# Performance work log

Hardware: AMD Instinct MI355X
Metric: run time of the kernel (lower is better)

Reference implementation:

```python
import jax, jax.numpy as jnp
import numpy as np

B, P, C = 8, 8192, 91            # images, proposals/image, classes (incl. background)
PRE_NMS_TOPK = 1000              # fixed-size candidate set per image for NMS
DET_PER_IMG = 100                # detections_per_img
SCORE_THRESH = 0.05
NMS_THRESH = 0.5
MIN_SIZE = 0.01                  # remove_small_boxes min_size
BBOX_W = (10.0, 10.0, 5.0, 5.0)  # bbox_reg_weights
BBOX_XFORM_CLIP = float(np.log(1000.0 / 16.0))
NEG = -1e9


def setup_inputs() -> dict:
    key = jax.random.key(0)
    k1, k2, k3, k4, k5, k6 = jax.random.split(key, 6)
    H, W = 800, 1333
    class_logits = jax.random.normal(k1, (B, P, C), jnp.float32)
    box_regression = jax.random.normal(k2, (B, P, 4 * C), jnp.float32) * 0.5
    # random valid proposal boxes inside the image
    cx = jax.random.uniform(k3, (B, P)) * W
    cy = jax.random.uniform(k4, (B, P)) * H
    bw = jax.random.uniform(k5, (B, P)) * 200.0 + 16.0
    bh = jax.random.uniform(k6, (B, P)) * 200.0 + 16.0
    x1 = jnp.clip(cx - 0.5 * bw, 0.0, W - 1.0)
    y1 = jnp.clip(cy - 0.5 * bh, 0.0, H - 1.0)
    x2 = jnp.clip(cx + 0.5 * bw, x1 + 1.0, float(W))
    y2 = jnp.clip(cy + 0.5 * bh, y1 + 1.0, float(H))
    proposals = jnp.stack([x1, y1, x2, y2], axis=-1)
    image_hw = jnp.array([H, W], jnp.int32)
    return {"class_logits": class_logits, "box_regression": box_regression,
            "proposals": proposals, "image_hw": image_hw}


def _iou_matrix(b):
    # b: [K,4] -> [K,K] pairwise IoU
    area = (b[:, 2] - b[:, 0]) * (b[:, 3] - b[:, 1])
    lt = jnp.maximum(b[:, None, :2], b[None, :, :2])
    rb = jnp.minimum(b[:, None, 2:], b[None, :, 2:])
    wh = jnp.clip(rb - lt, 0.0)
    inter = wh[..., 0] * wh[..., 1]
    return inter / (area[:, None] + area[None, :] - inter + 1e-9)


def _postprocess(class_logits, box_regression, proposals, image_hw):
    Hf = image_hw[0].astype(jnp.float32)
    Wf = image_hw[1].astype(jnp.float32)
    wx, wy, ww, wh = BBOX_W
    # --- BoxCoder.decode ---
    widths = proposals[..., 2] - proposals[..., 0]            # [B,P]
    heights = proposals[..., 3] - proposals[..., 1]
    ctr_x = proposals[..., 0] + 0.5 * widths
    ctr_y = proposals[..., 1] + 0.5 * heights
    rel = box_regression.reshape(B, P, C, 4)
    dx = rel[..., 0] / wx
    dy = rel[..., 1] / wy
    dw = jnp.minimum(rel[..., 2] / ww, BBOX_XFORM_CLIP)
    dh = jnp.minimum(rel[..., 3] / wh, BBOX_XFORM_CLIP)
    pcx = dx * widths[..., None] + ctr_x[..., None]           # [B,P,C]
    pcy = dy * heights[..., None] + ctr_y[..., None]
    pw = jnp.exp(dw) * widths[..., None]
    ph = jnp.exp(dh) * heights[..., None]
    # --- clip_boxes_to_image ---
    x1 = jnp.clip(pcx - 0.5 * pw, 0.0, Wf)
    y1 = jnp.clip(pcy - 0.5 * ph, 0.0, Hf)
    x2 = jnp.clip(pcx + 0.5 * pw, 0.0, Wf)
    y2 = jnp.clip(pcy + 0.5 * ph, 0.0, Hf)
    boxes = jnp.stack([x1, y1, x2, y2], axis=-1)              # [B,P,C,4]
    scores = jax.nn.softmax(class_logits, axis=-1)            # [B,P,C]
    # drop background class 0, flatten (proposal, class) candidates
    M = P * (C - 1)
    boxes_f = boxes[:, :, 1:, :].reshape(B, M, 4)
    scores_f = scores[:, :, 1:].reshape(B, M)
    labels_f = jnp.broadcast_to(jnp.tile(jnp.arange(1, C, dtype=jnp.int32), P), (B, M))
    # score threshold + remove_small_boxes as score masking (fixed shapes)
    ws = boxes_f[..., 2] - boxes_f[..., 0]
    hs = boxes_f[..., 3] - boxes_f[..., 1]
    valid = (scores_f > SCORE_THRESH) & (ws >= MIN_SIZE) & (hs >= MIN_SIZE)
    mscores = jnp.where(valid, scores_f, NEG)
    offset_scale = jnp.maximum(Hf, Wf) + 1.0

    def per_image(b, s, l):
        # pre-NMS top-k candidates (sorted descending, matching NMS score order)
        sk, idx = jax.lax.top_k(s, PRE_NMS_TOPK)              # [K]
        bk = b[idx]                                           # [K,4]
        lk = l[idx]
        valid_k = sk > NEG / 2
        # batched_nms via per-class coordinate offsets
        bo = bk + (lk.astype(jnp.float32) * offset_scale)[:, None]
        iou = _iou_matrix(bo)                                 # [K,K]
        K = PRE_NMS_TOPK
        rng = jnp.arange(K)
        def body(i, supp):
            active = jnp.logical_and(jnp.logical_not(supp[i]), valid_k[i])
            new = active & (iou[i] > NMS_THRESH) & (rng > i)
            return supp | new
        supp = jax.lax.fori_loop(0, K, body, jnp.zeros((K,), bool))
        keep = jnp.logical_and(jnp.logical_not(supp), valid_k)
        fs = jnp.where(keep, sk, NEG)
        fsd, fidx = jax.lax.top_k(fs, DET_PER_IMG)
        fb = bk[fidx]
        fl = lk[fidx]
        ok = fsd > NEG / 2
        return (jnp.where(ok[:, None], fb, 0.0),
                jnp.where(ok, fsd, 0.0),
                jnp.where(ok, fl, 0))

    return jax.vmap(per_image)(boxes_f, mscores, labels_f)


def reference(class_logits, box_regression, proposals, image_hw):
    boxes, scores, labels = _postprocess(class_logits, box_regression, proposals, image_hw)
    return boxes, scores, labels  # [B,100,4] float, [B,100] float, [B,100] int32
```

## Files before the change

kernel.cpp:

```cpp
#include <hip/hip_runtime.h>

namespace {

constexpr int NB = 8, NP = 8192, NC = 91;
constexpr int KTOP = 1000, NDET = 100;
constexpr int MROWS = 1024;
constexpr int NBUCK = 4096, SORTN = 4096;
constexpr int NLAB = 90;
constexpr int SHARDS = 32;
constexpr int SHCAP = 4864;
constexpr float SCORE_T = 0.05f;
constexpr float MIN_SZ = 0.01f;
constexpr float NMS_T = 0.5f;
constexpr float CLIPV = 4.135166556742356f;
constexpr float NEGV = -1e9f;

typedef unsigned long long ull;

__device__ __forceinline__ void decode_box(const float4& pr, const float4& rel,
                                           float Wf, float Hf,
                                           float& x1, float& y1, float& x2, float& y2) {
  float w = pr.z - pr.x, h = pr.w - pr.y;
  float cx = pr.x + 0.5f * w, cy = pr.y + 0.5f * h;
  float dx = rel.x / 10.0f, dy = rel.y / 10.0f;
  float dw = fminf(rel.z / 5.0f, CLIPV), dh = fminf(rel.w / 5.0f, CLIPV);
  float pcx = dx * w + cx, pcy = dy * h + cy;
  float pw = expf(dw) * w, ph = expf(dh) * h;
  x1 = fminf(fmaxf(pcx - 0.5f * pw, 0.0f), Wf);
  y1 = fminf(fmaxf(pcy - 0.5f * ph, 0.0f), Hf);
  x2 = fminf(fmaxf(pcx + 0.5f * pw, 0.0f), Wf);
  y2 = fminf(fmaxf(pcy + 0.5f * ph, 0.0f), Hf);
}

__device__ __forceinline__ int score_bucket(unsigned bits) {
  return min((int)((bits - 0x3D000000u) >> 14), NBUCK - 1);
}

__global__ __launch_bounds__(256) void k_candidates(
    const float* __restrict__ logits, const float* __restrict__ boxreg,
    const float* __restrict__ props, const int* __restrict__ hw,
    ull* __restrict__ dense, int* __restrict__ shcnt) {
  __shared__ float sh[16 * NC];
  __shared__ ull stage[16][20];
  __shared__ int gcnt[16];
  __shared__ int gbase[16];
  int tid = threadIdx.x;
  int base = blockIdx.x * 16;
  const float4* src4 = reinterpret_cast<const float4*>(logits + (size_t)base * NC);
  float4* sh4 = reinterpret_cast<float4*>(sh);
  for (int i = tid; i < (16 * NC) / 4; i += 256) sh4[i] = src4[i];
  __syncthreads();

  int lane = tid & 63;
  int l16 = lane & 15;
  int grp = lane >> 4;
  int wv = tid >> 6;
  int lp = wv * 4 + grp;
  int gw = base + lp;
  int b = gw >> 13;
  int p = gw & (NP - 1);
  float Hf = (float)hw[0], Wf = (float)hw[1];
  const float* row = sh + lp * NC;

  float zreg[6];
  float m = -3.0e38f;
#pragma unroll
  for (int k = 0; k < 6; ++k) {
    int c = k * 16 + l16;
    float z = (c < NC) ? row[c] : -3.0e38f;
    zreg[k] = z;
    m = fmaxf(m, z);
  }
#pragma unroll
  for (int d = 1; d < 16; d <<= 1) m = fmaxf(m, __shfl_xor(m, d, 64));
  float S = 0.0f;
#pragma unroll
  for (int k = 0; k < 6; ++k) {
    int c = k * 16 + l16;
    S += (c < NC) ? expf(zreg[k] - m) : 0.0f;
  }
#pragma unroll
  for (int d = 1; d < 16; d <<= 1) S += __shfl_xor(S, d, 64);

  float invS = 1.0f / S;
  float thr = m + logf(SCORE_T * S) - 1e-3f;

  float4 pr = reinterpret_cast<const float4*>(props)[gw];
  const float4* relrow = reinterpret_cast<const float4*>(boxreg + (size_t)gw * 4 * NC);
  unsigned below = (1u << l16) - 1u;
  int n = 0;
#pragma unroll
  for (int k = 0; k < 6; ++k) {
    int c = k * 16 + l16;
    bool ok = (c >= 1) && (c < NC) && (zreg[k] > thr);
    float sc = 0.0f;
    if (ok) {
      sc = expf(zreg[k] - m) * invS;
      ok = sc > SCORE_T;
      if (ok) {
        float4 rel = relrow[c];
        float x1, y1, x2, y2;
        decode_box(pr, rel, Wf, Hf, x1, y1, x2, y2);
        ok = ((x2 - x1) >= MIN_SZ) && ((y2 - y1) >= MIN_SZ);
      }
    }
    ull bal = __ballot(ok);
    unsigned gm = (unsigned)((bal >> (grp * 16)) & 0xFFFFull);
    if (ok) {
      int pos = n + __popc(gm & below);
      unsigned bits = __float_as_uint(sc);
      int idx = p * (NC - 1) + (c - 1);
      if (pos < 20) stage[lp][pos] = ((ull)bits << 32) | (unsigned)(~(unsigned)idx);
    }
    n += __popc(gm);
  }
  if (l16 == 0) gcnt[lp] = min(n, 20);
  __syncthreads();
  int shard = blockIdx.x & (SHARDS - 1);
  if (tid == 0) {
    int off[16];
    int tot = 0;
#pragma unroll
    for (int g = 0; g < 16; ++g) { off[g] = tot; tot += gcnt[g]; }
    int bs = tot ? atomicAdd(&shcnt[b * SHARDS + shard], tot) : 0;
#pragma unroll
    for (int g = 0; g < 16; ++g) gbase[g] = bs + off[g];
  }
  __syncthreads();
  ull* dst = dense + (size_t)(b * SHARDS + shard) * SHCAP;
  for (int j = l16; j < gcnt[lp]; j += 16) dst[gbase[lp] + j] = stage[lp][j];
}

__global__ __launch_bounds__(1024) void k_select(
    const ull* __restrict__ dense, const int* __restrict__ shcnt,
    const float* __restrict__ boxreg, const float* __restrict__ props,
    const int* __restrict__ hw,
    float* __restrict__ topk_score, float* __restrict__ det_box,
    int* __restrict__ det_label, int* __restrict__ keep, int* __restrict__ nvalid) {
  __shared__ int h[NBUCK];
  __shared__ int cur[NBUCK];
  __shared__ ull sk[SORTN];
  __shared__ int sbs;
  int b = blockIdx.x, tid = threadIdx.x;
#pragma unroll
  for (int k = 0; k < NBUCK / 1024; ++k) h[tid + k * 1024] = 0;
  if (tid == 0) sbs = 0;
  __syncthreads();
  for (int s = 0; s < SHARDS; ++s) {
    int cnt = shcnt[b * SHARDS + s];
    const ull* seg = dense + (size_t)(b * SHARDS + s) * SHCAP;
    for (int i = tid; i < cnt; i += 1024)
      atomicAdd(&h[score_bucket((unsigned)(seg[i] >> 32))], 1);
  }
  __syncthreads();
  for (int d = 1; d < NBUCK; d <<= 1) {
    int v[NBUCK / 1024];
#pragma unroll
    for (int k = 0; k < NBUCK / 1024; ++k) {
      int i = tid + k * 1024;
      v[k] = h[i] + ((i + d < NBUCK) ? h[i + d] : 0);
    }
    __syncthreads();
#pragma unroll
    for (int k = 0; k < NBUCK / 1024; ++k) h[tid + k * 1024] = v[k];
    __syncthreads();
  }
#pragma unroll
  for (int k = 0; k < NBUCK / 1024; ++k) {
    int i = tid + k * 1024;
    if (h[i] >= KTOP && (i == NBUCK - 1 || h[i + 1] < KTOP)) sbs = i;
  }
  __syncthreads();
#pragma unroll
  for (int k = 0; k < NBUCK / 1024; ++k) {
    int i = tid + k * 1024;
    cur[i] = (i + 1 < NBUCK) ? h[i + 1] : 0;
  }
  __syncthreads();
  int sb = sbs;
  int total = min(h[sb], SORTN);
  for (int s = 0; s < SHARDS; ++s) {
    int cnt = shcnt[b * SHARDS + s];
    const ull* seg = dense + (size_t)(b * SHARDS + s) * SHCAP;
    for (int i = tid; i < cnt; i += 1024) {
      ull key = seg[i];
      int bk = score_bucket((unsigned)(key >> 32));
      if (bk < sb) continue;
      int pos = atomicAdd(&cur[bk], 1);
      if (pos < SORTN) sk[pos] = key;
    }
  }
  __syncthreads();
  float Hf = (float)hw[0], Wf = (float)hw[1];
  for (int i = tid; i < total; i += 1024) {
    ull key = sk[i];
    int bk = score_bucket((unsigned)(key >> 32));
    int s0 = (bk + 1 < NBUCK) ? h[bk + 1] : 0;
    int e = min(cur[bk], total);
    int r = s0;
    for (int j = s0; j < e; ++j) r += (sk[j] > key) ? 1 : 0;
    if (r < KTOP) {
      int og = b * KTOP + r;
      topk_score[og] = __uint_as_float((unsigned)(key >> 32));
      int fidx = (int)(~(unsigned)key);
      int p = fidx / (NC - 1), c = fidx % (NC - 1) + 1;
      float4 pr = reinterpret_cast<const float4*>(props)[b * NP + p];
      float4 rel =
          reinterpret_cast<const float4*>(boxreg + (size_t)(b * NP + p) * 4 * NC)[c];
      float x1, y1, x2, y2;
      decode_box(pr, rel, Wf, Hf, x1, y1, x2, y2);
      det_box[(size_t)og * 4 + 0] = x1;
      det_box[(size_t)og * 4 + 1] = y1;
      det_box[(size_t)og * 4 + 2] = x2;
      det_box[(size_t)og * 4 + 3] = y2;
      det_label[og] = c;
      keep[og] = 1;
    }
  }
  int valid_n = min(total, KTOP);
  for (int r = valid_n + tid; r < KTOP; r += 1024) {
    int og = b * KTOP + r;
    topk_score[og] = NEGV;
    det_box[(size_t)og * 4 + 0] = 0.0f;
    det_box[(size_t)og * 4 + 1] = 0.0f;
    det_box[(size_t)og * 4 + 2] = 0.0f;
    det_box[(size_t)og * 4 + 3] = 0.0f;
    det_label[og] = 0;
    keep[og] = 0;
  }
  if (tid == 0) nvalid[b] = valid_n;
}

__global__ __launch_bounds__(64) void k_nms(
    const int* __restrict__ nvalid, const float* __restrict__ det_box,
    const int* __restrict__ det_label, int* __restrict__ keep) {
  __shared__ int list[MROWS];
  __shared__ float4 mbx[64];
  __shared__ unsigned char sup[MROWS];
  int bb = blockIdx.x;
  int b = bb / NLAB;
  int lab = bb % NLAB + 1;
  int lane = threadIdx.x;
  int nv = nvalid[b];
  ull below = (1ull << lane) - 1ull;
  const int* ll = det_label + b * KTOP;
  int c = 0;
  for (int base = 0; base < KTOP; base += 64) {
    int i = base + lane;
    bool mb = (i < KTOP) && (i < nv) && (ll[i] == lab);
    ull bal = __ballot(mb);
    if (mb) list[c + __popcll(bal & below)] = i;
    c += __popcll(bal);
  }
  if (c <= 1) return;
  __syncthreads();
  const float4* bbx = reinterpret_cast<const float4*>(det_box) + (size_t)b * KTOP;
  if (c <= 64) {
    if (lane < c) mbx[lane] = bbx[list[lane]];
    __syncthreads();
    float4 bx = mbx[(lane < c) ? lane : 0];
    float area = (bx.z - bx.x) * (bx.w - bx.y);
    ull col = 0ull;
    for (int i = 0; i + 1 < c; ++i) {
      float4 bi = mbx[i];
      float ai = (bi.z - bi.x) * (bi.w - bi.y);
      float ltx = fmaxf(bi.x, bx.x), lty = fmaxf(bi.y, bx.y);
      float rbx = fminf(bi.z, bx.z), rby = fminf(bi.w, bx.w);
      float iw = fmaxf(rbx - ltx, 0.0f), ih = fmaxf(rby - lty, 0.0f);
      float inter = iw * ih;
      float iou = inter / (ai + area - inter + 1e-9f);
      if ((lane > i) && (lane < c) && (iou > NMS_T)) col |= (1ull << i);
    }
    if (__ballot(col != 0ull)) {
      unsigned s = 0u;
      for (int i = 0; i + 1 < c; ++i) {
        ull act = __ballot(s == 0u);
        s |= (unsigned)((act >> i) & (col >> i) & 1ull);
      }
      if (lane < c && s) keep[b * KTOP + list[lane]] = 0;
    }
  } else {
    if (lane == 0) {
      for (int a = 0; a < c; ++a) sup[a] = 0;
      for (int a = 0; a < c; ++a) {
        if (sup[a]) continue;
        float4 bi = bbx[list[a]];
        float ai = (bi.z - bi.x) * (bi.w - bi.y);
        for (int e = a + 1; e < c; ++e) {
          if (sup[e]) continue;
          float4 bj = bbx[list[e]];
          float aj = (bj.z - bj.x) * (bj.w - bj.y);
          float ltx = fmaxf(bi.x, bj.x), lty = fmaxf(bi.y, bj.y);
          float rbx = fminf(bi.z, bj.z), rby = fminf(bi.w, bj.w);
          float iw = fmaxf(rbx - ltx, 0.0f), ih = fmaxf(rby - lty, 0.0f);
          float inter = iw * ih;
          if (inter / (ai + aj - inter + 1e-9f) > NMS_T) sup[e] = 1;
        }
      }
      for (int a = 0; a < c; ++a)
        if (sup[a]) keep[b * KTOP + list[a]] = 0;
    }
  }
}

__global__ __launch_bounds__(256) void k_output(
    const float* __restrict__ topk_score, const float* __restrict__ det_box,
    const int* __restrict__ det_label, const int* __restrict__ keep,
    float* __restrict__ out) {
  __shared__ int kp[MROWS];
  __shared__ int pf[MROWS];
  int b = blockIdx.x, tid = threadIdx.x;
  for (int i = tid; i < MROWS; i += 256) {
    int v = (i < KTOP) ? keep[b * KTOP + i] : 0;
    kp[i] = v;
    pf[i] = v;
  }
  __syncthreads();
  for (int d = 1; d < MROWS; d <<= 1) {
    int v[4];
#pragma unroll
    for (int k = 0; k < 4; ++k) {
      int i = tid + k * 256;
      v[k] = pf[i] + ((i >= d) ? pf[i - d] : 0);
    }
    __syncthreads();
#pragma unroll
    for (int k = 0; k < 4; ++k) pf[tid + k * 256] = v[k];
    __syncthreads();
  }
  int total = min(pf[KTOP - 1], NDET);
  float* ob = out;
  float* os = out + (size_t)NB * NDET * 4;
  float* ol = os + (size_t)NB * NDET;
  for (int i = tid; i < KTOP; i += 256) {
    if (kp[i]) {
      int r = pf[i] - 1;
      if (r < NDET) {
        ob[((size_t)b * NDET + r) * 4 + 0] = det_box[((size_t)b * KTOP + i) * 4 + 0];
        ob[((size_t)b * NDET + r) * 4 + 1] = det_box[((size_t)b * KTOP + i) * 4 + 1];
        ob[((size_t)b * NDET + r) * 4 + 2] = det_box[((size_t)b * KTOP + i) * 4 + 2];
        ob[((size_t)b * NDET + r) * 4 + 3] = det_box[((size_t)b * KTOP + i) * 4 + 3];
        os[b * NDET + r] = topk_score[b * KTOP + i];
        ol[b * NDET + r] = (float)det_label[b * KTOP + i];
      }
    }
  }
  for (int r = total + tid; r < NDET; r += 256) {
    ob[((size_t)b * NDET + r) * 4 + 0] = 0.0f;
    ob[((size_t)b * NDET + r) * 4 + 1] = 0.0f;
    ob[((size_t)b * NDET + r) * 4 + 2] = 0.0f;
    ob[((size_t)b * NDET + r) * 4 + 3] = 0.0f;
    os[b * NDET + r] = 0.0f;
    ol[b * NDET + r] = 0.0f;
  }
}

}

extern "C" void kernel_launch(void* const* d_in, const int* in_sizes, int n_in,
                              void* d_out, int out_size, void* d_ws, size_t ws_size,
                              hipStream_t stream) {
  const float* logits = (const float*)d_in[0];
  const float* boxreg = (const float*)d_in[1];
  const float* props = (const float*)d_in[2];
  const int* hw = (const int*)d_in[3];

  char* ws = (char*)d_ws;
  size_t off = 0;
  auto alloc = [&](size_t bytes) -> void* {
    void* p = ws + off;
    off += (bytes + 255) & ~(size_t)255;
    return p;
  };
  ull* dense = (ull*)alloc((size_t)NB * SHARDS * SHCAP * 8);
  int* shcnt = (int*)alloc((size_t)NB * SHARDS * 4);
  float* topk_score = (float*)alloc((size_t)NB * KTOP * 4);
  float* det_box = (float*)alloc((size_t)NB * KTOP * 16);
  int* det_label = (int*)alloc((size_t)NB * KTOP * 4);
  int* keep = (int*)alloc((size_t)NB * KTOP * 4);
  int* nvalid = (int*)alloc(NB * 4);

  hipMemsetAsync(shcnt, 0, (size_t)NB * SHARDS * 4, stream);
  k_candidates<<<(NB * NP) / 16, 256, 0, stream>>>(logits, boxreg, props, hw,
                                                   dense, shcnt);
  k_select<<<NB, 1024, 0, stream>>>(dense, shcnt, boxreg, props, hw,
                                    topk_score, det_box, det_label, keep, nvalid);
  k_nms<<<NB * NLAB, 64, 0, stream>>>(nvalid, det_box, det_label, keep);
  k_output<<<NB, 256, 0, stream>>>(topk_score, det_box, det_label, keep, (float*)d_out);
}
```

Baseline: 77.59 us.

## Replace atomic shard compaction with per-block fixed-slot candidate buffers

Each candidate block now writes its survivors into its own fixed-capacity slot and records a per-block count, instead of reserving space in 32 shared shards per image with global atomics. This removes the global atomicAdd contention and the memset launch. In the select kernel, each pair of threads now walks one block's segment, replacing the loop over shards. The trade-off is uneven per-thread work in k_select, since segment counts vary, and reads that are less coalesced than contiguous shard scans.

```diff
diff --git a/kernel.cpp b/kernel.cpp
--- a/kernel.cpp
+++ b/kernel.cpp
@@ -7,8 +7,8 @@
 constexpr int MROWS = 1024;
 constexpr int NBUCK = 4096, SORTN = 4096;
 constexpr int NLAB = 90;
-constexpr int SHARDS = 32;
-constexpr int SHCAP = 4864;
+constexpr int BPI = 512;
+constexpr int BCAP = 304;
 constexpr float SCORE_T = 0.05f;
 constexpr float MIN_SZ = 0.01f;
 constexpr float NMS_T = 0.5f;
@@ -39,7 +39,7 @@
 __global__ __launch_bounds__(256) void k_candidates(
     const float* __restrict__ logits, const float* __restrict__ boxreg,
     const float* __restrict__ props, const int* __restrict__ hw,
-    ull* __restrict__ dense, int* __restrict__ shcnt) {
+    ull* __restrict__ dense, int* __restrict__ bcnt) {
   __shared__ float sh[16 * NC];
   __shared__ ull stage[16][20];
   __shared__ int gcnt[16];
@@ -57,7 +57,6 @@
   int wv = tid >> 6;
   int lp = wv * 4 + grp;
   int gw = base + lp;
-  int b = gw >> 13;
   int p = gw & (NP - 1);
   float Hf = (float)hw[0], Wf = (float)hw[1];
   const float* row = sh + lp * NC;
@@ -116,23 +115,22 @@
   }
   if (l16 == 0) gcnt[lp] = min(n, 20);
   __syncthreads();
-  int shard = blockIdx.x & (SHARDS - 1);
   if (tid == 0) {
     int off[16];
     int tot = 0;
 #pragma unroll
     for (int g = 0; g < 16; ++g) { off[g] = tot; tot += gcnt[g]; }
-    int bs = tot ? atomicAdd(&shcnt[b * SHARDS + shard], tot) : 0;
-#pragma unroll
-    for (int g = 0; g < 16; ++g) gbase[g] = bs + off[g];
-  }
-  __syncthreads();
-  ull* dst = dense + (size_t)(b * SHARDS + shard) * SHCAP;
+#pragma unroll
+    for (int g = 0; g < 16; ++g) gbase[g] = off[g];
+    bcnt[blockIdx.x] = tot;
+  }
+  __syncthreads();
+  ull* dst = dense + (size_t)blockIdx.x * BCAP;
   for (int j = l16; j < gcnt[lp]; j += 16) dst[gbase[lp] + j] = stage[lp][j];
 }
 
 __global__ __launch_bounds__(1024) void k_select(
-    const ull* __restrict__ dense, const int* __restrict__ shcnt,
+    const ull* __restrict__ dense, const int* __restrict__ bcnt,
     const float* __restrict__ boxreg, const float* __restrict__ props,
     const int* __restrict__ hw,
     float* __restrict__ topk_score, float* __restrict__ det_box,
@@ -146,12 +144,13 @@
   for (int k = 0; k < NBUCK / 1024; ++k) h[tid + k * 1024] = 0;
   if (tid == 0) sbs = 0;
   __syncthreads();
-  for (int s = 0; s < SHARDS; ++s) {
-    int cnt = shcnt[b * SHARDS + s];
-    const ull* seg = dense + (size_t)(b * SHARDS + s) * SHCAP;
-    for (int i = tid; i < cnt; i += 1024)
-      atomicAdd(&h[score_bucket((unsigned)(seg[i] >> 32))], 1);
-  }
+  int seg = tid >> 1;
+  int par = tid & 1;
+  int gseg = b * BPI + seg;
+  int scnt = bcnt[gseg];
+  const ull* sptr = dense + (size_t)gseg * BCAP;
+  for (int j = par; j < scnt; j += 2)
+    atomicAdd(&h[score_bucket((unsigned)(sptr[j] >> 32))], 1);
   __syncthreads();
   for (int d = 1; d < NBUCK; d <<= 1) {
     int v[NBUCK / 1024];
@@ -179,16 +178,12 @@
   __syncthreads();
   int sb = sbs;
   int total = min(h[sb], SORTN);
-  for (int s = 0; s < SHARDS; ++s) {
-    int cnt = shcnt[b * SHARDS + s];
-    const ull* seg = dense + (size_t)(b * SHARDS + s) * SHCAP;
-    for (int i = tid; i < cnt; i += 1024) {
-      ull key = seg[i];
-      int bk = score_bucket((unsigned)(key >> 32));
-      if (bk < sb) continue;
-      int pos = atomicAdd(&cur[bk], 1);
-      if (pos < SORTN) sk[pos] = key;
-    }
+  for (int j = par; j < scnt; j += 2) {
+    ull key = sptr[j];
+    int bk = score_bucket((unsigned)(key >> 32));
+    if (bk < sb) continue;
+    int pos = atomicAdd(&cur[bk], 1);
+    if (pos < SORTN) sk[pos] = key;
   }
   __syncthreads();
   float Hf = (float)hw[0], Wf = (float)hw[1];
@@ -372,18 +367,17 @@
     off += (bytes + 255) & ~(size_t)255;
     return p;
   };
-  ull* dense = (ull*)alloc((size_t)NB * SHARDS * SHCAP * 8);
-  int* shcnt = (int*)alloc((size_t)NB * SHARDS * 4);
+  ull* dense = (ull*)alloc((size_t)NB * BPI * BCAP * 8);
+  int* bcnt = (int*)alloc((size_t)NB * BPI * 4);
   float* topk_score = (float*)alloc((size_t)NB * KTOP * 4);
   float* det_box = (float*)alloc((size_t)NB * KTOP * 16);
   int* det_label = (int*)alloc((size_t)NB * KTOP * 4);
   int* keep = (int*)alloc((size_t)NB * KTOP * 4);
   int* nvalid = (int*)alloc(NB * 4);
 
-  hipMemsetAsync(shcnt, 0, (size_t)NB * SHARDS * 4, stream);
   k_candidates<<<(NB * NP) / 16, 256, 0, stream>>>(logits, boxreg, props, hw,
-                                                   dense, shcnt);
-  k_select<<<NB, 1024, 0, stream>>>(dense, shcnt, boxreg, props, hw,
+                                                   dense, bcnt);
+  k_select<<<NB, 1024, 0, stream>>>(dense, bcnt, boxreg, props, hw,
                                     topk_score, det_box, det_label, keep, nvalid);
   k_nms<<<NB * NLAB, 64, 0, stream>>>(nvalid, det_box, det_label, keep);
   k_output<<<NB, 256, 0, stream>>>(topk_score, det_box, det_label, keep, (float*)d_out);
```

New measurement: 62.48 us, median of 3. -19.5%, faster.
